# Performance work log

Hardware: AMD Instinct MI355X
Metric: run time of the kernel (lower is better)

## Reference

```python
import jax, jax.numpy as jnp
import numpy as np

N, E, R = 50000, 800000, 3
D, H = 128, 128
NUM_SHAPE, NUM_COLOR, MAX_POS = 16, 8, 25
B, NUM_CLASS = 256, 10
EPS = 1e-5


def setup_inputs() -> dict:
    key = jax.random.key(0)
    ks = jax.random.split(key, 24)
    s = lambda fan: 1.0 / np.sqrt(fan)
    inp = {
        "x_idx": jax.random.randint(ks[0], (N, 3), 0, 8),
        "edge_index": jax.random.randint(ks[1], (2, E), 0, N),
        "edge_type": jax.random.randint(ks[2], (E,), 0, R),
        "batch": jnp.sort(jax.random.randint(ks[3], (N,), 0, B)),
        "shape_emb": jax.random.normal(ks[4], (NUM_SHAPE, D), jnp.float32),
        "color_emb": jax.random.normal(ks[5], (NUM_COLOR, D), jnp.float32),
        "pos_emb": jax.random.normal(ks[6], (MAX_POS, D), jnp.float32),
        "W1": jax.random.normal(ks[7], (R, D, H), jnp.float32) * s(D),
        "root1": jax.random.normal(ks[8], (D, H), jnp.float32) * s(D),
        "b1": jax.random.normal(ks[9], (H,), jnp.float32) * 0.01,
        "g1": jax.random.uniform(ks[10], (H,), jnp.float32, 0.5, 1.5),
        "beta1": jax.random.normal(ks[11], (H,), jnp.float32) * 0.1,
        "m1": jax.random.normal(ks[12], (H,), jnp.float32) * 0.1,
        "v1": jax.random.uniform(ks[13], (H,), jnp.float32, 0.5, 1.5),
        "W2": jax.random.normal(ks[14], (R, H, H), jnp.float32) * s(H),
        "root2": jax.random.normal(ks[15], (H, H), jnp.float32) * s(H),
        "b2": jax.random.normal(ks[16], (H,), jnp.float32) * 0.01,
        "g2": jax.random.uniform(ks[17], (H,), jnp.float32, 0.5, 1.5),
        "beta2": jax.random.normal(ks[18], (H,), jnp.float32) * 0.1,
        "m2": jax.random.normal(ks[19], (H,), jnp.float32) * 0.1,
        "v2": jax.random.uniform(ks[20], (H,), jnp.float32, 0.5, 1.5),
        "clsW": jax.random.normal(ks[21], (H, NUM_CLASS), jnp.float32) * s(H),
        "clsb": jax.random.normal(ks[22], (NUM_CLASS,), jnp.float32) * 0.01,
    }
    return inp


def rgcn_conv(x, edge_index, edge_type, W, root, b):
    # per-relation transform, gather at src, mean-scatter at dst (PyG RGCNConv, aggr='mean')
    src, dst = edge_index[0], edge_index[1]
    xw = jnp.einsum('nd,rdh->rnh', x, W)            # [R, N, H]
    msg = xw[edge_type, src]                        # [E, H]
    seg = dst * R + edge_type                       # segment per (dst, relation)
    ssum = jax.ops.segment_sum(msg, seg, num_segments=N * R)
    cnt = jax.ops.segment_sum(jnp.ones((E,), x.dtype), seg, num_segments=N * R)
    mean = jnp.where(cnt[:, None] > 0, ssum / jnp.maximum(cnt, 1.0)[:, None], 0.0)
    agg = mean.reshape(N, R, -1).sum(axis=1)        # sum over relations of per-relation means
    return agg + x @ root + b


def batchnorm_eval(x, g, beta, m, v):
    return g * (x - m) * jax.lax.rsqrt(v + EPS) + beta


def reference(x_idx, edge_index, edge_type, batch, shape_emb, color_emb, pos_emb,
              W1, root1, b1, g1, beta1, m1, v1,
              W2, root2, b2, g2, beta2, m2, v2, clsW, clsb):
    x = (shape_emb[x_idx[:, 0]] + color_emb[x_idx[:, 1]]
         + pos_emb[jnp.clip(x_idx[:, 2], 0, MAX_POS - 1)])
    x = jax.nn.relu(batchnorm_eval(rgcn_conv(x, edge_index, edge_type, W1, root1, b1),
                                   g1, beta1, m1, v1))
    x = jax.nn.relu(batchnorm_eval(rgcn_conv(x, edge_index, edge_type, W2, root2, b2),
                                   g2, beta2, m2, v2))
    hsum = jax.ops.segment_sum(x, batch, num_segments=B)
    hcnt = jax.ops.segment_sum(jnp.ones((N,), x.dtype), batch, num_segments=B)
    hg = hsum / jnp.maximum(hcnt, 1.0)[:, None]     # global mean pool [B, H]
    return hg @ clsW + clsb
```

## Files before the change

### kernel.cpp

```cpp
#include <hip/hip_runtime.h>

#define N_NODES 50000
#define E_EDGES 800000
#define R_REL 3
#define NSEG (N_NODES * R_REL)
#define DH 128
#define KDIM 512
#define ROWB 1024
#define XOFF (3 * DH * 2)
#define BATCHES 256
#define NCLASS 10
#define EPSV 1e-5f

#define BSHIFT 7
#define BNODES 128
#define NBUCK ((N_NODES + BNODES - 1) / BNODES)
#define SEGB (BNODES * R_REL)
#define CAP 4096

typedef __attribute__((ext_vector_type(8))) short short8v;
typedef __attribute__((ext_vector_type(4))) unsigned uint4v;
typedef __attribute__((ext_vector_type(4))) float float4v;
typedef unsigned short ushort_t;

__device__ __forceinline__ ushort_t f2bf(float f) {
    union { float f; unsigned u; } x; x.f = f;
    unsigned r = x.u + 0x7FFFu + ((x.u >> 16) & 1u);
    return (ushort_t)(r >> 16);
}
__device__ __forceinline__ float bf2f(ushort_t h) {
    union { unsigned u; float f; } x; x.u = ((unsigned)h) << 16;
    return x.f;
}
__device__ __forceinline__ float u2f(unsigned u) {
    union { unsigned u; float f; } x; x.u = u;
    return x.f;
}

__global__ void build_x_kernel(const int* __restrict__ xi,
                               const float* __restrict__ se,
                               const float* __restrict__ ce,
                               const float* __restrict__ pe,
                               ushort_t* __restrict__ A) {
    int tid = blockIdx.x * blockDim.x + threadIdx.x;
    int node = tid >> 4, c = tid & 15;
    if (node >= N_NODES) return;
    int i0 = xi[node * 3 + 0];
    int i1 = xi[node * 3 + 1];
    int i2 = xi[node * 3 + 2];
    i2 = i2 < 0 ? 0 : (i2 > 24 ? 24 : i2);
    const float4* sa = reinterpret_cast<const float4*>(se + (size_t)i0 * DH + c * 8);
    const float4* sb = reinterpret_cast<const float4*>(ce + (size_t)i1 * DH + c * 8);
    const float4* sp = reinterpret_cast<const float4*>(pe + (size_t)i2 * DH + c * 8);
    short8v o;
    #pragma unroll
    for (int q = 0; q < 2; ++q) {
        float4 a = sa[q], b = sb[q], p = sp[q];
        o[q * 4 + 0] = (short)f2bf(a.x + b.x + p.x);
        o[q * 4 + 1] = (short)f2bf(a.y + b.y + p.y);
        o[q * 4 + 2] = (short)f2bf(a.z + b.z + p.z);
        o[q * 4 + 3] = (short)f2bf(a.w + b.w + p.w);
    }
    *reinterpret_cast<short8v*>(A + (size_t)node * KDIM + 3 * DH + c * 8) = o;
}

__global__ __launch_bounds__(256) void hist_kernel(const int* __restrict__ ei,
                                                   int* __restrict__ bcount) {
    __shared__ int lh[NBUCK];
    for (int i = threadIdx.x; i < NBUCK; i += 256) lh[i] = 0;
    __syncthreads();
    int stride = gridDim.x * 256;
    for (int e = blockIdx.x * 256 + threadIdx.x; e < E_EDGES; e += stride)
        atomicAdd(&lh[ei[E_EDGES + e] >> BSHIFT], 1);
    __syncthreads();
    for (int i = threadIdx.x; i < NBUCK; i += 256)
        if (lh[i]) atomicAdd(&bcount[i], lh[i]);
}

__global__ __launch_bounds__(512) void bucket_scan_kernel(const int* __restrict__ bcount,
                                                          int* __restrict__ bbase,
                                                          int* __restrict__ bcur,
                                                          int* __restrict__ offs3) {
    __shared__ int sh[512];
    int t = threadIdx.x;
    int v = (t < NBUCK) ? bcount[t] : 0;
    sh[t] = v;
    __syncthreads();
    for (int d = 1; d < 512; d <<= 1) {
        int u = (t >= d) ? sh[t - d] : 0;
        __syncthreads();
        sh[t] += u;
        __syncthreads();
    }
    int excl = sh[t] - v;
    if (t < NBUCK) { bbase[t] = excl; bcur[t * 16] = excl; }
    if (t == NBUCK - 1) bbase[NBUCK] = sh[t];
    if (t == 0) offs3[NSEG] = E_EDGES;
}

__global__ void append_kernel(const int* __restrict__ ei, const int* __restrict__ et,
                              int* __restrict__ bcur, int* __restrict__ tlist) {
    int e = blockIdx.x * blockDim.x + threadIdx.x;
    if (e >= E_EDGES) return;
    int src = ei[e];
    int dst = ei[E_EDGES + e];
    int r = et[e];
    int b = dst >> BSHIFT;
    int ls = (dst & (BNODES - 1)) * R_REL + r;
    int pos = atomicAdd(&bcur[b * 16], 1);
    tlist[pos] = (ls << 16) | src;
}

__global__ __launch_bounds__(512) void localsort_kernel(const int* __restrict__ tlist,
                                                        const int* __restrict__ bbase,
                                                        int* __restrict__ offs3,
                                                        int* __restrict__ elist) {
    __shared__ int hist[512];
    __shared__ int tl[CAP];
    __shared__ int el[CAP];
    int b = blockIdx.x, t = threadIdx.x;
    int ebeg = bbase[b], eend = bbase[b + 1];
    int cnt = eend - ebeg;
    int segbase = b * SEGB;
    hist[t] = 0;
    __syncthreads();

    if (cnt <= CAP) {
        for (int i = t; i < cnt; i += 512) {
            int pk = tlist[ebeg + i];
            tl[i] = pk;
            atomicAdd(&hist[pk >> 16], 1);
        }
        __syncthreads();
        int v = hist[t];
        for (int d = 1; d < 512; d <<= 1) {
            int u = (t >= d) ? hist[t - d] : 0;
            __syncthreads();
            hist[t] += u;
            __syncthreads();
        }
        int excl = hist[t] - v;
        if (t < SEGB && segbase + t < NSEG) offs3[segbase + t] = ebeg + excl;
        __syncthreads();
        hist[t] = excl;
        __syncthreads();
        for (int i = t; i < cnt; i += 512) {
            int pk = tl[i];
            int pos = atomicAdd(&hist[pk >> 16], 1);
            el[pos] = (pk & 0xFFFF) * ROWB + XOFF;
        }
        __syncthreads();
        for (int i = t; i < cnt; i += 512)
            elist[ebeg + i] = el[i];
    } else {
        for (int i = t; i < cnt; i += 512)
            atomicAdd(&hist[tlist[ebeg + i] >> 16], 1);
        __syncthreads();
        int v = hist[t];
        for (int d = 1; d < 512; d <<= 1) {
            int u = (t >= d) ? hist[t - d] : 0;
            __syncthreads();
            hist[t] += u;
            __syncthreads();
        }
        int excl = hist[t] - v;
        if (t < SEGB && segbase + t < NSEG) offs3[segbase + t] = ebeg + excl;
        __syncthreads();
        hist[t] = excl;
        __syncthreads();
        for (int i = t; i < cnt; i += 512) {
            int pk = tlist[ebeg + i];
            int pos = atomicAdd(&hist[pk >> 16], 1);
            elist[ebeg + pos] = (pk & 0xFFFF) * ROWB + XOFF;
        }
    }
}

__global__ void setup_kernel(const float* __restrict__ W1, const float* __restrict__ root1,
                             const float* __restrict__ W2, const float* __restrict__ root2,
                             ushort_t* __restrict__ Wf1, ushort_t* __restrict__ Wf2,
                             const int* __restrict__ batch, int* __restrict__ bstart,
                             const float* __restrict__ b1, const float* __restrict__ g1,
                             const float* __restrict__ be1, const float* __restrict__ m1,
                             const float* __restrict__ v1,
                             const float* __restrict__ b2, const float* __restrict__ g2,
                             const float* __restrict__ be2, const float* __restrict__ m2,
                             const float* __restrict__ v2,
                             float* __restrict__ sc1, float* __restrict__ sh1,
                             float* __restrict__ sc2, float* __restrict__ sh2) {
    int tid = blockIdx.x * blockDim.x + threadIdx.x;
    if (tid < 16384) {
        int L = tid >> 13;
        int rem = tid & 8191;
        int l = rem & 63;
        int nt = (rem >> 6) & 7;
        int ks = rem >> 9;
        const float* W = L ? W2 : W1;
        const float* root = L ? root2 : root1;
        ushort_t* dst = (L ? Wf2 : Wf1) + (size_t)rem * 8;
        int col = nt * 16 + (l & 15);
        int kb = ks * 32 + (l >> 4) * 8;
        short8v o;
        #pragma unroll
        for (int j = 0; j < 8; ++j) {
            int k = kb + j;
            float w = (k < 384) ? W[(size_t)k * DH + col] : root[(size_t)(k - 384) * DH + col];
            o[j] = (short)f2bf(w);
        }
        *reinterpret_cast<short8v*>(dst) = o;
    } else if (tid < 16384 + BATCHES + 1) {
        int b = tid - 16384;
        int lo = 0, hi = N_NODES;
        while (lo < hi) {
            int mid = (lo + hi) >> 1;
            if (batch[mid] < b) lo = mid + 1; else hi = mid;
        }
        bstart[b] = lo;
    } else if (tid < 16384 + 257 + DH) {
        int c = tid - 16384 - 257;
        float s = g1[c] * rsqrtf(v1[c] + EPSV);
        sc1[c] = s;
        sh1[c] = (b1[c] - m1[c]) * s + be1[c];
    } else if (tid < 16384 + 257 + 2 * DH) {
        int c = tid - 16384 - 257 - DH;
        float s = g2[c] * rsqrtf(v2[c] + EPSV);
        sc2[c] = s;
        sh2[c] = (b2[c] - m2[c]) * s + be2[c];
    }
}

__global__ __launch_bounds__(256) void agg_kernel(const char* __restrict__ Ab,
                                                  const int* __restrict__ offs3,
                                                  const int* __restrict__ elist,
                                                  char* __restrict__ Aob) {
    int t = threadIdx.x;
    int g = t >> 4, c = t & 15;
    int n = blockIdx.x * 16 + g;
    if (n >= N_NODES) return;
    int s0 = offs3[3 * n + 0];
    int s1 = offs3[3 * n + 1];
    int s2 = offs3[3 * n + 2];
    int s3 = offs3[3 * n + 3];
    int cb = c * 16;

    float r0l0 = 0, r0h0 = 0, r0l1 = 0, r0h1 = 0, r0l2 = 0, r0h2 = 0, r0l3 = 0, r0h3 = 0;
    float r1l0 = 0, r1h0 = 0, r1l1 = 0, r1h1 = 0, r1l2 = 0, r1h2 = 0, r1l3 = 0, r1h3 = 0;
    float r2l0 = 0, r2h0 = 0, r2l1 = 0, r2h1 = 0, r2l2 = 0, r2h2 = 0, r2l3 = 0, r2h3 = 0;

    #define RUN_SEG(BEG, END, L0, H0, L1, H1, L2, H2, L3, H3)                        \
    {                                                                                \
        int i = (BEG);                                                               \
        uint4v v0, v1;                                                               \
        if (i < (END))                                                               \
            v0 = *reinterpret_cast<const uint4v*>(Ab + elist[i] + cb);               \
        if (i + 1 < (END))                                                           \
            v1 = *reinterpret_cast<const uint4v*>(Ab + elist[i + 1] + cb);           \
        for (; i < (END); ++i) {                                                     \
            uint4v v2;                                                               \
            if (i + 2 < (END))                                                       \
                v2 = *reinterpret_cast<const uint4v*>(Ab + elist[i + 2] + cb);       \
            L0 += u2f(v0[0] << 16); H0 += u2f(v0[0] & 0xFFFF0000u);                  \
            L1 += u2f(v0[1] << 16); H1 += u2f(v0[1] & 0xFFFF0000u);                  \
            L2 += u2f(v0[2] << 16); H2 += u2f(v0[2] & 0xFFFF0000u);                  \
            L3 += u2f(v0[3] << 16); H3 += u2f(v0[3] & 0xFFFF0000u);                  \
            v0 = v1; v1 = v2;                                                        \
        }                                                                            \
    }

    RUN_SEG(s0, s1, r0l0, r0h0, r0l1, r0h1, r0l2, r0h2, r0l3, r0h3)
    RUN_SEG(s1, s2, r1l0, r1h0, r1l1, r1h1, r1l2, r1h2, r1l3, r1h3)
    RUN_SEG(s2, s3, r2l0, r2h0, r2l1, r2h1, r2l2, r2h2, r2l3, r2h3)
    #undef RUN_SEG

    int c0 = s1 - s0, c1 = s2 - s1, c2 = s3 - s2;
    float i0 = c0 ? 1.f / c0 : 0.f;
    float i1 = c1 ? 1.f / c1 : 0.f;
    float i2 = c2 ? 1.f / c2 : 0.f;
    char* base = Aob + (size_t)n * ROWB + cb;
    uint4v o;
    o[0] = (unsigned)f2bf(r0l0 * i0) | ((unsigned)f2bf(r0h0 * i0) << 16);
    o[1] = (unsigned)f2bf(r0l1 * i0) | ((unsigned)f2bf(r0h1 * i0) << 16);
    o[2] = (unsigned)f2bf(r0l2 * i0) | ((unsigned)f2bf(r0h2 * i0) << 16);
    o[3] = (unsigned)f2bf(r0l3 * i0) | ((unsigned)f2bf(r0h3 * i0) << 16);
    *reinterpret_cast<uint4v*>(base + 0 * 256) = o;
    o[0] = (unsigned)f2bf(r1l0 * i1) | ((unsigned)f2bf(r1h0 * i1) << 16);
    o[1] = (unsigned)f2bf(r1l1 * i1) | ((unsigned)f2bf(r1h1 * i1) << 16);
    o[2] = (unsigned)f2bf(r1l2 * i1) | ((unsigned)f2bf(r1h2 * i1) << 16);
    o[3] = (unsigned)f2bf(r1l3 * i1) | ((unsigned)f2bf(r1h3 * i1) << 16);
    *reinterpret_cast<uint4v*>(base + 1 * 256) = o;
    o[0] = (unsigned)f2bf(r2l0 * i2) | ((unsigned)f2bf(r2h0 * i2) << 16);
    o[1] = (unsigned)f2bf(r2l1 * i2) | ((unsigned)f2bf(r2h1 * i2) << 16);
    o[2] = (unsigned)f2bf(r2l2 * i2) | ((unsigned)f2bf(r2h2 * i2) << 16);
    o[3] = (unsigned)f2bf(r2l3 * i2) | ((unsigned)f2bf(r2h3 * i2) << 16);
    *reinterpret_cast<uint4v*>(base + 2 * 256) = o;
}

__global__ __launch_bounds__(256) void gemm_mfma_kernel(const ushort_t* __restrict__ A,
                                                        const ushort_t* __restrict__ Wf,
                                                        const float* __restrict__ sc,
                                                        const float* __restrict__ sh,
                                                        ushort_t* __restrict__ Aout) {
    int w = threadIdx.x >> 6, l = threadIdx.x & 63;
    int base = blockIdx.x * 64 + w * 16;
    int arow = base + (l & 15);
    if (arow >= N_NODES) arow = N_NODES - 1;
    const short8v* ap = reinterpret_cast<const short8v*>(A + (size_t)arow * KDIM + (l >> 4) * 8);
    const short8v* wf = reinterpret_cast<const short8v*>(Wf) + l;

    float4v acc[8];
    #pragma unroll
    for (int nt = 0; nt < 8; ++nt) acc[nt] = (float4v){0.f, 0.f, 0.f, 0.f};

    #pragma unroll 4
    for (int ks = 0; ks < 16; ++ks) {
        short8v a = ap[ks * 4];
        const short8v* bp = wf + ks * 512;
        #pragma unroll
        for (int nt = 0; nt < 8; ++nt) {
            short8v b = bp[nt * 64];
            acc[nt] = __builtin_amdgcn_mfma_f32_16x16x32_bf16(a, b, acc[nt], 0, 0, 0);
        }
    }

    int colb = l & 15;
    int rowq = (l >> 4) * 4;
    #pragma unroll
    for (int nt = 0; nt < 8; ++nt) {
        int col = nt * 16 + colb;
        float scv = sc[col], shv = sh[col];
        #pragma unroll
        for (int r = 0; r < 4; ++r) {
            int row = base + rowq + r;
            if (row < N_NODES) {
                float val = fmaxf(acc[nt][r] * scv + shv, 0.f);
                Aout[(size_t)row * KDIM + 3 * DH + col] = f2bf(val);
            }
        }
    }
}

__global__ __launch_bounds__(256) void pool_cls_kernel(
        const ushort_t* __restrict__ h,
        const int* __restrict__ bstart,
        const float* __restrict__ clsW,
        const float* __restrict__ clsb,
        float* __restrict__ out) {
    __shared__ float hsh[DH];
    int b = blockIdx.x;
    int t = threadIdx.x;
    int c = t & 127;
    int half = t >> 7;
    int beg = bstart[b], end = bstart[b + 1];
    float s = 0.f;
    for (int n = beg + half; n < end; n += 2)
        s += bf2f(h[(size_t)n * KDIM + c]);
    if (half == 1) hsh[c] = s;
    __syncthreads();
    if (half == 0) {
        float cnt = (float)(end - beg);
        float inv = cnt > 0.f ? 1.f / cnt : 1.f;
        hsh[c] = (s + hsh[c]) * inv;
    }
    __syncthreads();
    if (t < NCLASS) {
        float acc = clsb[t];
        #pragma unroll 16
        for (int d = 0; d < DH; ++d)
            acc += hsh[d] * clsW[d * NCLASS + t];
        out[b * NCLASS + t] = acc;
    }
}

extern "C" void kernel_launch(void* const* d_in, const int* in_sizes, int n_in,
                              void* d_out, int out_size, void* d_ws, size_t ws_size,
                              hipStream_t stream) {
    const int*   x_idx  = (const int*)d_in[0];
    const int*   eidx   = (const int*)d_in[1];
    const int*   etype  = (const int*)d_in[2];
    const int*   batch  = (const int*)d_in[3];
    const float* se     = (const float*)d_in[4];
    const float* ce     = (const float*)d_in[5];
    const float* pe     = (const float*)d_in[6];
    const float* W1     = (const float*)d_in[7];
    const float* root1  = (const float*)d_in[8];
    const float* b1     = (const float*)d_in[9];
    const float* g1     = (const float*)d_in[10];
    const float* beta1  = (const float*)d_in[11];
    const float* m1     = (const float*)d_in[12];
    const float* v1     = (const float*)d_in[13];
    const float* W2     = (const float*)d_in[14];
    const float* root2  = (const float*)d_in[15];
    const float* b2     = (const float*)d_in[16];
    const float* g2     = (const float*)d_in[17];
    const float* beta2  = (const float*)d_in[18];
    const float* m2     = (const float*)d_in[19];
    const float* v2     = (const float*)d_in[20];
    const float* clsW   = (const float*)d_in[21];
    const float* clsb   = (const float*)d_in[22];
    float* out = (float*)d_out;

    char* ws = (char*)d_ws;
    const size_t A_bytes     = (size_t)N_NODES * KDIM * 2;
    const size_t elist_bytes = (size_t)E_EDGES * 4;
    const size_t tlist_bytes = (size_t)E_EDGES * 4;
    const size_t offs3_pad   = 600064;
    ushort_t* A      = (ushort_t*)(ws);
    int*      elist  = (int*)(ws + A_bytes);
    int*      tlist  = (int*)(ws + A_bytes + elist_bytes);
    int*      offs3  = (int*)(ws + A_bytes + elist_bytes + tlist_bytes);
    char*     p      = ws + A_bytes + elist_bytes + tlist_bytes + offs3_pad;
    int*      bcount = (int*)p;            p += 1600;
    int*      bbase  = (int*)p;            p += 1600;
    int*      bcur   = (int*)p;            p += NBUCK * 64;
    int*      bstart = (int*)p;            p += 1088;
    ushort_t* Wf1    = (ushort_t*)p;       p += 131072;
    ushort_t* Wf2    = (ushort_t*)p;       p += 131072;
    float*    sc1    = (float*)p;          p += 512;
    float*    sh1    = (float*)p;          p += 512;
    float*    sc2    = (float*)p;          p += 512;
    float*    sh2    = (float*)p;          p += 512;

    const int TB = 256;

    hipMemsetAsync(bcount, 0, NBUCK * 4, stream);

    build_x_kernel<<<(N_NODES * 16 + TB - 1) / TB, TB, 0, stream>>>(x_idx, se, ce, pe, A);

    setup_kernel<<<67, 256, 0, stream>>>(W1, root1, W2, root2, Wf1, Wf2,
                                         batch, bstart,
                                         b1, g1, beta1, m1, v1,
                                         b2, g2, beta2, m2, v2,
                                         sc1, sh1, sc2, sh2);

    hist_kernel<<<64, 256, 0, stream>>>(eidx, bcount);
    bucket_scan_kernel<<<1, 512, 0, stream>>>(bcount, bbase, bcur, offs3);
    append_kernel<<<(E_EDGES + TB - 1) / TB, TB, 0, stream>>>(eidx, etype, bcur, tlist);
    localsort_kernel<<<NBUCK, 512, 0, stream>>>(tlist, bbase, offs3, elist);

    agg_kernel<<<(N_NODES + 15) / 16, 256, 0, stream>>>((const char*)A, offs3, elist, (char*)A);
    gemm_mfma_kernel<<<(N_NODES + 63) / 64, 256, 0, stream>>>(A, Wf1, sc1, sh1, A);

    agg_kernel<<<(N_NODES + 15) / 16, 256, 0, stream>>>((const char*)A, offs3, elist, (char*)A);
    gemm_mfma_kernel<<<(N_NODES + 63) / 64, 256, 0, stream>>>(A, Wf2, sc2, sh2, A);

    pool_cls_kernel<<<BATCHES, 256, 0, stream>>>(A + 3 * DH, bstart, clsW, clsb, out);
}
```

Measured before the change: 268.1 us.

## Replace atomic bucket append with chunked counting-sort scatter and larger buckets

Edge bucketing now uses a per-chunk histogram matrix, a single-block scan, and a per-chunk local sort in shared memory. Each chunk then writes its contiguous runs into the bucket positions. This removes the global atomic append on bucket cursors, which was contended, and the memset. Buckets grow from 128 to 512 nodes with a larger shared-memory capacity, so localsort has far fewer blocks, each with more shared memory, which may lower occupancy.

After: 235.2 us. 12.3% less time.

```diff
diff --git a/kernel.cpp b/kernel.cpp
--- a/kernel.cpp
+++ b/kernel.cpp
@@ -12,11 +12,14 @@
 #define NCLASS 10
 #define EPSV 1e-5f
 
-#define BSHIFT 7
-#define BNODES 128
+#define BSHIFT 9
+#define BNODES 512
 #define NBUCK ((N_NODES + BNODES - 1) / BNODES)
 #define SEGB (BNODES * R_REL)
-#define CAP 4096
+#define CAP 9216
+#define NCHUNK 128
+#define CHUNK (E_EDGES / NCHUNK)
+#define MATN (NBUCK * NCHUNK)
 
 typedef __attribute__((ext_vector_type(8))) short short8v;
 typedef __attribute__((ext_vector_type(4))) unsigned uint4v;
@@ -64,86 +67,154 @@
     *reinterpret_cast<short8v*>(A + (size_t)node * KDIM + 3 * DH + c * 8) = o;
 }
 
-__global__ __launch_bounds__(256) void hist_kernel(const int* __restrict__ ei,
-                                                   int* __restrict__ bcount) {
+__global__ __launch_bounds__(512) void chunk_hist_kernel(const int* __restrict__ ei,
+                                                         int* __restrict__ mat) {
     __shared__ int lh[NBUCK];
-    for (int i = threadIdx.x; i < NBUCK; i += 256) lh[i] = 0;
-    __syncthreads();
-    int stride = gridDim.x * 256;
-    for (int e = blockIdx.x * 256 + threadIdx.x; e < E_EDGES; e += stride)
-        atomicAdd(&lh[ei[E_EDGES + e] >> BSHIFT], 1);
-    __syncthreads();
-    for (int i = threadIdx.x; i < NBUCK; i += 256)
-        if (lh[i]) atomicAdd(&bcount[i], lh[i]);
-}
-
-__global__ __launch_bounds__(512) void bucket_scan_kernel(const int* __restrict__ bcount,
-                                                          int* __restrict__ bbase,
-                                                          int* __restrict__ bcur,
-                                                          int* __restrict__ offs3) {
-    __shared__ int sh[512];
+    int t = threadIdx.x, blk = blockIdx.x;
+    if (t < NBUCK) lh[t] = 0;
+    __syncthreads();
+    int base = blk * CHUNK;
+    for (int i = t; i < CHUNK; i += 512)
+        atomicAdd(&lh[ei[E_EDGES + base + i] >> BSHIFT], 1);
+    __syncthreads();
+    if (t < NBUCK) mat[t * NCHUNK + blk] = lh[t];
+}
+
+__global__ __launch_bounds__(1024) void matscan_kernel(int* __restrict__ mat,
+                                                       int* __restrict__ bbase,
+                                                       int* __restrict__ offs3) {
+    __shared__ int partial[1024];
     int t = threadIdx.x;
-    int v = (t < NBUCK) ? bcount[t] : 0;
-    sh[t] = v;
-    __syncthreads();
-    for (int d = 1; d < 512; d <<= 1) {
-        int u = (t >= d) ? sh[t - d] : 0;
-        __syncthreads();
-        sh[t] += u;
-        __syncthreads();
-    }
-    int excl = sh[t] - v;
-    if (t < NBUCK) { bbase[t] = excl; bcur[t * 16] = excl; }
-    if (t == NBUCK - 1) bbase[NBUCK] = sh[t];
-    if (t == 0) offs3[NSEG] = E_EDGES;
-}
-
-__global__ void append_kernel(const int* __restrict__ ei, const int* __restrict__ et,
-                              int* __restrict__ bcur, int* __restrict__ tlist) {
-    int e = blockIdx.x * blockDim.x + threadIdx.x;
-    if (e >= E_EDGES) return;
-    int src = ei[e];
-    int dst = ei[E_EDGES + e];
-    int r = et[e];
-    int b = dst >> BSHIFT;
-    int ls = (dst & (BNODES - 1)) * R_REL + r;
-    int pos = atomicAdd(&bcur[b * 16], 1);
-    tlist[pos] = (ls << 16) | src;
+    int buf[13];
+    int base = t * 13;
+    int s = 0;
+    #pragma unroll
+    for (int j = 0; j < 13; ++j) {
+        int idx = base + j;
+        int v = (idx < MATN) ? mat[idx] : 0;
+        buf[j] = s;
+        s += v;
+    }
+    partial[t] = s;
+    __syncthreads();
+    for (int d = 1; d < 1024; d <<= 1) {
+        int u = (t >= d) ? partial[t - d] : 0;
+        __syncthreads();
+        partial[t] += u;
+        __syncthreads();
+    }
+    int off = (t > 0) ? partial[t - 1] : 0;
+    #pragma unroll
+    for (int j = 0; j < 13; ++j) {
+        int idx = base + j;
+        if (idx < MATN) mat[idx] = off + buf[j];
+    }
+    __syncthreads();
+    if (t < NBUCK) bbase[t] = mat[t * NCHUNK];
+    if (t == 0) { bbase[NBUCK] = E_EDGES; offs3[NSEG] = E_EDGES; }
+}
+
+__global__ __launch_bounds__(512) void chunk_scatter_kernel(const int* __restrict__ ei,
+                                                            const int* __restrict__ et,
+                                                            const int* __restrict__ mat,
+                                                            int* __restrict__ tlist) {
+    __shared__ int sorted[CHUNK];
+    __shared__ int lh[NBUCK];
+    __shared__ int lstart[NBUCK + 1];
+    __shared__ int mbase[NBUCK];
+    __shared__ int scr[128];
+    int t = threadIdx.x, blk = blockIdx.x;
+    if (t < NBUCK) { lh[t] = 0; mbase[t] = mat[t * NCHUNK + blk]; }
+    __syncthreads();
+    int base = blk * CHUNK;
+    for (int i = t; i < CHUNK; i += 512)
+        atomicAdd(&lh[ei[E_EDGES + base + i] >> BSHIFT], 1);
+    __syncthreads();
+    if (t < 128) scr[t] = (t < NBUCK) ? lh[t] : 0;
+    __syncthreads();
+    for (int d = 1; d < 128; d <<= 1) {
+        int u = 0;
+        if (t < 128 && t >= d) u = scr[t - d];
+        __syncthreads();
+        if (t < 128) scr[t] += u;
+        __syncthreads();
+    }
+    if (t < NBUCK) lstart[t] = scr[t] - lh[t];
+    if (t == NBUCK - 1) lstart[NBUCK] = scr[t];
+    __syncthreads();
+    if (t < NBUCK) lh[t] = lstart[t];
+    __syncthreads();
+    for (int i = t; i < CHUNK; i += 512) {
+        int e = base + i;
+        int src = ei[e];
+        int dst = ei[E_EDGES + e];
+        int r = et[e];
+        int b = dst >> BSHIFT;
+        int ls = (dst & (BNODES - 1)) * R_REL + r;
+        int p = atomicAdd(&lh[b], 1);
+        sorted[p] = (ls << 16) | src;
+    }
+    __syncthreads();
+    for (int i = t; i < CHUNK; i += 512) {
+        int lo = 0, hi = NBUCK - 1;
+        while (lo < hi) {
+            int mid = (lo + hi + 1) >> 1;
+            if (lstart[mid] <= i) lo = mid; else hi = mid - 1;
+        }
+        tlist[mbase[lo] + (i - lstart[lo])] = sorted[i];
+    }
 }
 
 __global__ __launch_bounds__(512) void localsort_kernel(const int* __restrict__ tlist,
                                                         const int* __restrict__ bbase,
                                                         int* __restrict__ offs3,
                                                         int* __restrict__ elist) {
-    __shared__ int hist[512];
+    __shared__ int hist[SEGB];
+    __shared__ int scr[512];
     __shared__ int tl[CAP];
     __shared__ int el[CAP];
     int b = blockIdx.x, t = threadIdx.x;
     int ebeg = bbase[b], eend = bbase[b + 1];
     int cnt = eend - ebeg;
     int segbase = b * SEGB;
-    hist[t] = 0;
-    __syncthreads();
-
-    if (cnt <= CAP) {
+    #pragma unroll
+    for (int j = 0; j < 3; ++j) hist[t + j * 512] = 0;
+    __syncthreads();
+
+    bool fit = (cnt <= CAP);
+    if (fit) {
         for (int i = t; i < cnt; i += 512) {
             int pk = tlist[ebeg + i];
             tl[i] = pk;
             atomicAdd(&hist[pk >> 16], 1);
         }
-        __syncthreads();
-        int v = hist[t];
-        for (int d = 1; d < 512; d <<= 1) {
-            int u = (t >= d) ? hist[t - d] : 0;
-            __syncthreads();
-            hist[t] += u;
-            __syncthreads();
-        }
-        int excl = hist[t] - v;
-        if (t < SEGB && segbase + t < NSEG) offs3[segbase + t] = ebeg + excl;
-        __syncthreads();
-        hist[t] = excl;
-        __syncthreads();
+    } else {
+        for (int i = t; i < cnt; i += 512)
+            atomicAdd(&hist[tlist[ebeg + i] >> 16], 1);
+    }
+    __syncthreads();
+    int h0 = hist[3 * t], h1 = hist[3 * t + 1], h2 = hist[3 * t + 2];
+    int s = h0 + h1 + h2;
+    scr[t] = s;
+    __syncthreads();
+    for (int d = 1; d < 512; d <<= 1) {
+        int u = (t >= d) ? scr[t - d] : 0;
+        __syncthreads();
+        scr[t] += u;
+        __syncthreads();
+    }
+    int off = (t > 0) ? scr[t - 1] : 0;
+    int e0 = off, e1 = off + h0, e2 = off + h0 + h1;
+    {
+        int sg = segbase + 3 * t;
+        if (sg < NSEG)     offs3[sg]     = ebeg + e0;
+        if (sg + 1 < NSEG) offs3[sg + 1] = ebeg + e1;
+        if (sg + 2 < NSEG) offs3[sg + 2] = ebeg + e2;
+    }
+    __syncthreads();
+    hist[3 * t] = e0; hist[3 * t + 1] = e1; hist[3 * t + 2] = e2;
+    __syncthreads();
+    if (fit) {
         for (int i = t; i < cnt; i += 512) {
             int pk = tl[i];
             int pos = atomicAdd(&hist[pk >> 16], 1);
@@ -153,21 +224,6 @@
         for (int i = t; i < cnt; i += 512)
             elist[ebeg + i] = el[i];
     } else {
-        for (int i = t; i < cnt; i += 512)
-            atomicAdd(&hist[tlist[ebeg + i] >> 16], 1);
-        __syncthreads();
-        int v = hist[t];
-        for (int d = 1; d < 512; d <<= 1) {
-            int u = (t >= d) ? hist[t - d] : 0;
-            __syncthreads();
-            hist[t] += u;
-            __syncthreads();
-        }
-        int excl = hist[t] - v;
-        if (t < SEGB && segbase + t < NSEG) offs3[segbase + t] = ebeg + excl;
-        __syncthreads();
-        hist[t] = excl;
-        __syncthreads();
         for (int i = t; i < cnt; i += 512) {
             int pk = tlist[ebeg + i];
             int pos = atomicAdd(&hist[pk >> 16], 1);
@@ -409,9 +465,8 @@
     int*      tlist  = (int*)(ws + A_bytes + elist_bytes);
     int*      offs3  = (int*)(ws + A_bytes + elist_bytes + tlist_bytes);
     char*     p      = ws + A_bytes + elist_bytes + tlist_bytes + offs3_pad;
-    int*      bcount = (int*)p;            p += 1600;
-    int*      bbase  = (int*)p;            p += 1600;
-    int*      bcur   = (int*)p;            p += NBUCK * 64;
+    int*      mat    = (int*)p;            p += 50176;
+    int*      bbase  = (int*)p;            p += 512;
     int*      bstart = (int*)p;            p += 1088;
     ushort_t* Wf1    = (ushort_t*)p;       p += 131072;
     ushort_t* Wf2    = (ushort_t*)p;       p += 131072;
@@ -422,8 +477,6 @@
 
     const int TB = 256;
 
-    hipMemsetAsync(bcount, 0, NBUCK * 4, stream);
-
     build_x_kernel<<<(N_NODES * 16 + TB - 1) / TB, TB, 0, stream>>>(x_idx, se, ce, pe, A);
 
     setup_kernel<<<67, 256, 0, stream>>>(W1, root1, W2, root2, Wf1, Wf2,
@@ -432,9 +485,9 @@
                                          b2, g2, beta2, m2, v2,
                                          sc1, sh1, sc2, sh2);
 
-    hist_kernel<<<64, 256, 0, stream>>>(eidx, bcount);
-    bucket_scan_kernel<<<1, 512, 0, stream>>>(bcount, bbase, bcur, offs3);
-    append_kernel<<<(E_EDGES + TB - 1) / TB, TB, 0, stream>>>(eidx, etype, bcur, tlist);
+    chunk_hist_kernel<<<NCHUNK, 512, 0, stream>>>(eidx, mat);
+    matscan_kernel<<<1, 1024, 0, stream>>>(mat, bbase, offs3);
+    chunk_scatter_kernel<<<NCHUNK, 512, 0, stream>>>(eidx, etype, mat, tlist);
     localsort_kernel<<<NBUCK, 512, 0, stream>>>(tlist, bbase, offs3, elist);
 
     agg_kernel<<<(N_NODES + 15) / 16, 256, 0, stream>>>((const char*)A, offs3, elist, (char*)A);
```
